# Optimization experiments

Hardware: AMD Instinct MI355X
Metric: run time of the kernel (lower is better)

## Reference

```python
import jax, jax.numpy as jnp
import numpy as np

BS, L, DIM = 16, 2048, 512
NUM_GROUPS, NUM_CODES = 2, 320
CODE_DIM = 256
VAR_DIM = CODE_DIM // NUM_GROUPS  # 128
INNER = DIM * 2                    # projFactor=2
TAU = 2.0                          # max(maxTemp*decay**0, minTemp) at numUpdates=0


def setup_inputs() -> dict:
    key = jax.random.key(0)
    ks = jax.random.split(key, 7)
    x = jax.random.normal(ks[0], (BS, L, DIM), jnp.float32)
    # gumbels = -log(Exp(1)) == standard Gumbel noise, matching torch's exponential_().log().neg()
    gumbels = jax.random.gumbel(ks[1], (BS * L * NUM_GROUPS, NUM_CODES), jnp.float32)
    W1 = jax.random.normal(ks[2], (DIM, INNER), jnp.float32) * (1.0 / np.sqrt(DIM))
    b1 = jnp.zeros((INNER,), jnp.float32)
    W2 = jax.random.normal(ks[3], (INNER, NUM_GROUPS * NUM_CODES), jnp.float32) * (1.0 / np.sqrt(INNER))
    b2 = jnp.zeros((NUM_GROUPS * NUM_CODES,), jnp.float32)
    # nn.init.uniform_ on embeddings: U[0,1); combineGroups=True -> single shared codebook (numCodes, varDim)
    emb = jax.random.uniform(ks[4], (NUM_CODES, VAR_DIM), jnp.float32)
    return {"x": x, "gumbels": gumbels, "W1": W1, "b1": b1, "W2": W2, "b2": b2, "emb": emb}


def reference(x, gumbels, W1, b1, W2, b2, emb):
    bs, l, d = x.shape
    xt = x.reshape(bs * l, d)
    h = jax.nn.gelu(xt @ W1 + b1, approximate=False)          # (N, INNER), torch GELU is exact erf
    logits = (h @ W2 + b2).reshape(bs * l * NUM_GROUPS, NUM_CODES)
    # training path: gumbel-softmax with straight-through hard one-hot
    soft = jax.nn.softmax((logits + gumbels) / TAU, axis=-1)  # (N*G, C)
    idx = jnp.argmax(soft, axis=-1)
    hard = jax.nn.one_hot(idx, NUM_CODES, dtype=soft.dtype)
    st = hard + soft - jax.lax.stop_gradient(soft)            # straight-through estimator
    st = st.reshape(bs * l, NUM_GROUPS, NUM_CODES)
    # combineGroups=True: embeddings repeated per group == shared codebook; the
    # (broadcast-mul).sum(-2) in torch is exactly this contraction (no huge intermediate).
    out = jnp.einsum('ngc,cd->ngd', st, emb)                  # (N, G, varDim)
    return out.reshape(bs, l, NUM_GROUPS * VAR_DIM)
```

## Files before the change

### kernel.cpp

```cpp
#include <hip/hip_runtime.h>
#include <math.h>


#define NTOK   32768
#define DIM    512
#define INNER  1024
#define NC     320
#define NGRP   2
#define VD     128
#define OUTD   256
#define RCAP   2048
#define MARGIN 8.0e-3f

#define L_LIST 16u
#define L_W1T  (64u<<10)
#define L_W2T  (2u<<20)
#define L_XH   (4u<<20)
#define L_H    (36u<<20)
#define L_PART (100u<<20)
#define L_HDW  (104u<<20)
#define WS_NEED (120u<<20)

#define W1F_OFF (1u<<20)
#define W2F_OFF (1u<<21)
#define SMEM_BYTES (65536 + 3328)

typedef _Float16 half8 __attribute__((ext_vector_type(8)));
typedef _Float16 half4 __attribute__((ext_vector_type(4)));
typedef float    f32x4 __attribute__((ext_vector_type(4)));

__device__ __forceinline__ float gelu_f(float s) {
  return 0.5f * s * (1.0f + erff(s * 0.70710678118654752440f));
}

#if defined(__has_builtin) && __has_builtin(__builtin_amdgcn_global_load_lds)
#define GLOAD16(gp, ldsbase) \
  __builtin_amdgcn_global_load_lds((const __attribute__((address_space(1))) void*)(gp), \
                                   (__attribute__((address_space(3))) void*)(ldsbase), 16, 0, 0)
#else
#define GLOAD16(gp, ldsbase) \
  do { *(uint4*)((char*)(ldsbase) + (threadIdx.x & 63) * 16) = *(const uint4*)(gp); } while (0)
#endif

#define XH_JOBS   2097152
#define W1T_JOBS  65536
#define W2T_JOBS  81920
#define PREP_JOBS (XH_JOBS + W1T_JOBS + W2T_JOBS)
__global__ __launch_bounds__(256)
void prep2_kernel(const float* __restrict__ x, const float* __restrict__ W1,
                  const float* __restrict__ W2, _Float16* __restrict__ xh,
                  _Float16* __restrict__ W1T, _Float16* __restrict__ W2T,
                  unsigned* __restrict__ cnt) {
  const int o = blockIdx.x * 256 + threadIdx.x;
  if (o == 0) cnt[0] = 0u;
  if (o < XH_JOBS) {
    const float4 v0 = *(const float4*)(x + (size_t)o * 8);
    const float4 v1 = *(const float4*)(x + (size_t)o * 8 + 4);
    half8 hv;
    hv[0] = (_Float16)v0.x; hv[1] = (_Float16)v0.y; hv[2] = (_Float16)v0.z; hv[3] = (_Float16)v0.w;
    hv[4] = (_Float16)v1.x; hv[5] = (_Float16)v1.y; hv[6] = (_Float16)v1.z; hv[7] = (_Float16)v1.w;
    *(half8*)(xh + (size_t)o * 8) = hv;
  } else if (o < XH_JOBS + W1T_JOBS) {
    const int q = o - XH_JOBS;
    const int i = q >> 6, k0 = (q & 63) * 8;
#pragma unroll
    for (int j = 0; j < 8; ++j)
      W1T[(size_t)i * DIM + k0 + j] = (_Float16)W1[(size_t)(k0 + j) * INNER + i];
  } else if (o < PREP_JOBS) {
    const int q = o - XH_JOBS - W1T_JOBS;
    const int c = q >> 7, i0 = (q & 127) * 8;
#pragma unroll
    for (int j = 0; j < 8; ++j)
      W2T[(size_t)c * INNER + i0 + j] = (_Float16)W2[(size_t)(i0 + j) * (NC * NGRP) + c];
  }
}

__global__ __launch_bounds__(256, 4)
void gemm1_kernel(const _Float16* __restrict__ xh, const _Float16* __restrict__ W1T,
                  const float* __restrict__ b1, _Float16* __restrict__ h) {
  __shared__ char smem[32768];
  const int tid = threadIdx.x;
  const int w = tid >> 6, l = tid & 63;
  const int l15 = l & 15, lq = l >> 4;
  const int bid = blockIdx.x;
  const int xcd = bid & 7, j = bid >> 3;
  const int bm = xcd * 32 + (j >> 3), bn = j & 7;
  const int wm = w >> 1, wn = w & 1;

  const int r0 = (w * 2 + 0) * 16 + (l >> 2);
  const int r1 = (w * 2 + 1) * 16 + (l >> 2);
  const int c0 = (((l & 3) ^ (r0 & 3)) * 8);
  const int c1 = (((l & 3) ^ (r1 & 3)) * 8);
  const _Float16* gA0 = xh  + (size_t)(bm * 128 + r0) * DIM + c0;
  const _Float16* gA1 = xh  + (size_t)(bm * 128 + r1) * DIM + c1;
  const _Float16* gB0 = W1T + (size_t)(bn * 128 + r0) * DIM + c0;
  const _Float16* gB1 = W1T + (size_t)(bn * 128 + r1) * DIM + c1;

#define STAGE_G(buf, ks) do { \
    char* b_ = smem + (buf) * 16384; \
    GLOAD16(gA0 + (ks) * 32, b_ + (w * 2 + 0) * 1024); \
    GLOAD16(gA1 + (ks) * 32, b_ + (w * 2 + 1) * 1024); \
    GLOAD16(gB0 + (ks) * 32, b_ + 8192 + (w * 2 + 0) * 1024); \
    GLOAD16(gB1 + (ks) * 32, b_ + 8192 + (w * 2 + 1) * 1024); \
  } while (0)

  f32x4 acc[4][4];
#pragma unroll
  for (int i = 0; i < 4; ++i)
#pragma unroll
    for (int jj = 0; jj < 4; ++jj) { f32x4 z = {0.f, 0.f, 0.f, 0.f}; acc[i][jj] = z; }

  const int swz = (lq ^ (l15 & 3)) << 4;
  const int aoff = (wm * 64 + l15) * 64 + swz;
  const int boff = 8192 + (wn * 64 + l15) * 64 + swz;

  STAGE_G(0, 0);
  __syncthreads();
  for (int ks = 0; ks < 16; ++ks) {
    const int cur = ks & 1;
    if (ks + 1 < 16) STAGE_G(cur ^ 1, ks + 1);
    const char* base = smem + cur * 16384;
    half8 a[4], b[4];
#pragma unroll
    for (int mi = 0; mi < 4; ++mi) a[mi] = *(const half8*)(base + aoff + mi * 1024);
#pragma unroll
    for (int ni = 0; ni < 4; ++ni) b[ni] = *(const half8*)(base + boff + ni * 1024);
#pragma unroll
    for (int mi = 0; mi < 4; ++mi)
#pragma unroll
      for (int ni = 0; ni < 4; ++ni)
        acc[mi][ni] = __builtin_amdgcn_mfma_f32_16x16x32_f16(a[mi], b[ni], acc[mi][ni], 0, 0, 0);
    __syncthreads();
  }

  _Float16* eT = (_Float16*)smem;
  float bb[4];
#pragma unroll
  for (int ni = 0; ni < 4; ++ni) bb[ni] = b1[bn * 128 + wn * 64 + ni * 16 + l15];
#pragma unroll
  for (int mi = 0; mi < 4; ++mi) {
    const int row = wm * 64 + mi * 16 + lq * 4;
#pragma unroll
    for (int ni = 0; ni < 4; ++ni) {
      const int col = (wn * 64 + ni * 16 + l15) ^ (lq << 4);
#pragma unroll
      for (int r = 0; r < 4; ++r)
        eT[(row + r) * 128 + col] = (_Float16)gelu_f(acc[mi][ni][r] + bb[ni]);
    }
  }
  __syncthreads();
#pragma unroll
  for (int it = 0; it < 8; ++it) {
    const int s = tid + it * 256;
    const int row = s >> 4, i8 = s & 15;
    const int colp = (i8 * 8) ^ (((row >> 2) & 3) << 4);
    *(half8*)(h + (size_t)(bm * 128 + row) * INNER + bn * 128 + i8 * 8)
        = *(const half8*)(eT + row * 128 + colp);
  }
}

__global__ __launch_bounds__(256, 4)
void gemm2_kernel(const _Float16* __restrict__ h, const _Float16* __restrict__ W2T,
                  const float* __restrict__ b2, const float* __restrict__ gum,
                  unsigned* __restrict__ part) {
  __shared__ char smem[32768];
  const int tid = threadIdx.x;
  const int w = tid >> 6, l = tid & 63;
  const int l15 = l & 15, lq = l >> 4;
  const int bid = blockIdx.x;
  const int xcd = bid & 7, j = bid >> 3;
  const int bm = xcd * 32 + j / 5, bt = j % 5;
  const int wm = w >> 1, wn = w & 1;

  const int r0 = (w * 2 + 0) * 16 + (l >> 2);
  const int r1 = (w * 2 + 1) * 16 + (l >> 2);
  const int c0 = (((l & 3) ^ (r0 & 3)) * 8);
  const int c1 = (((l & 3) ^ (r1 & 3)) * 8);
  const _Float16* gA0 = h   + (size_t)(bm * 128 + r0) * INNER + c0;
  const _Float16* gA1 = h   + (size_t)(bm * 128 + r1) * INNER + c1;
  const _Float16* gB0 = W2T + (size_t)(bt * 128 + r0) * INNER + c0;
  const _Float16* gB1 = W2T + (size_t)(bt * 128 + r1) * INNER + c1;

  f32x4 acc[4][4];
#pragma unroll
  for (int i = 0; i < 4; ++i)
#pragma unroll
    for (int jj = 0; jj < 4; ++jj) { f32x4 z = {0.f, 0.f, 0.f, 0.f}; acc[i][jj] = z; }

  const int swz = (lq ^ (l15 & 3)) << 4;
  const int aoff = (wm * 64 + l15) * 64 + swz;
  const int boff = 8192 + (wn * 64 + l15) * 64 + swz;

  STAGE_G(0, 0);
  __syncthreads();
  for (int ks = 0; ks < 32; ++ks) {
    const int cur = ks & 1;
    if (ks + 1 < 32) STAGE_G(cur ^ 1, ks + 1);
    const char* base = smem + cur * 16384;
    half8 a[4], b[4];
#pragma unroll
    for (int mi = 0; mi < 4; ++mi) a[mi] = *(const half8*)(base + aoff + mi * 1024);
#pragma unroll
    for (int ni = 0; ni < 4; ++ni) b[ni] = *(const half8*)(base + boff + ni * 1024);
#pragma unroll
    for (int mi = 0; mi < 4; ++mi)
#pragma unroll
      for (int ni = 0; ni < 4; ++ni)
        acc[mi][ni] = __builtin_amdgcn_mfma_f32_16x16x32_f16(a[mi], b[ni], acc[mi][ni], 0, 0, 0);
    __syncthreads();
  }

  float* eF = (float*)smem;
  const int nm = (bt == 2) ? 8 : 16;
#pragma unroll
  for (int half = 0; half < 2; ++half) {
    __syncthreads();
    if (wm == half) {
#pragma unroll
      for (int mi = 0; mi < 4; ++mi) {
        const int rl = mi * 16 + lq * 4;
#pragma unroll
        for (int ni = 0; ni < 4; ++ni) {
          const int col = (wn * 64 + ni * 16 + l15) ^ ((lq & 1) << 4);
#pragma unroll
          for (int r = 0; r < 4; ++r) eF[(rl + r) * 128 + col] = acc[mi][ni][r];
        }
      }
    }
    __syncthreads();
#pragma unroll
    for (int it = 0; it < 8; ++it) {
      const int s = tid + it * 256;
      const int rl = s >> 5, cc = (s & 31) * 4;
      const int ccp = cc ^ (((rl >> 2) & 1) << 4);
      const int t = bm * 128 + half * 64 + rl;
      const float4 lv  = *(const float4*)(eF + rl * 128 + ccp);
      const float4 b2v = *(const float4*)(b2 + bt * 128 + cc);
      const float4 gv  = *(const float4*)(gum + (size_t)t * 640 + bt * 128 + cc);
      float m1 = -1e30f, m2 = -1e30f; unsigned i1 = 0;
      const float vv[4] = {(lv.x + b2v.x) + gv.x, (lv.y + b2v.y) + gv.y,
                           (lv.z + b2v.z) + gv.z, (lv.w + b2v.w) + gv.w};
#pragma unroll
      for (int r = 0; r < 4; ++r) {
        const unsigned c = (unsigned)(bt * 128 + cc + r);
        if (vv[r] > m1) { m2 = m1; m1 = vv[r]; i1 = c; }
        else if (vv[r] > m2) m2 = vv[r];
      }
      for (int m = 1; m <= nm; m <<= 1) {
        const float om1 = __shfl_xor(m1, m);
        const float om2 = __shfl_xor(m2, m);
        const unsigned oi = (unsigned)__shfl_xor((int)i1, m);
        const bool take = (om1 > m1) || (om1 == m1 && oi < i1);
        if (take) { m2 = fmaxf(m1, om2); m1 = om1; i1 = oi; }
        else      { m2 = fmaxf(m2, om1); }
      }
      const int lr = tid & 31;
      const bool writer = (bt == 2) ? (lr == 0 || lr == 16) : (lr == 0);
      if (writer) {
        int slot;
        if (bt == 0) slot = 0; else if (bt == 1) slot = 1;
        else if (bt == 3) slot = 4; else if (bt == 4) slot = 5;
        else slot = (i1 < (unsigned)NC) ? 2 : 3;
        const unsigned ing = (i1 < (unsigned)NC) ? i1 : (i1 - NC);
        unsigned* p = part + ((size_t)t * 6 + slot) * 4;
        p[0] = __float_as_uint(m1);
        p[1] = __float_as_uint(m2);
        p[2] = ing;
      }
    }
  }
}

__global__ __launch_bounds__(256, 4)
void reduce_kernel(const unsigned* __restrict__ part, const float* __restrict__ emb,
                   float* __restrict__ out, unsigned* __restrict__ cnt,
                   unsigned* __restrict__ list) {
  __shared__ unsigned idxs[256];
  const int tid = threadIdx.x;
  const int pair = blockIdx.x * 256 + tid;
  const int t = pair >> 1, g = pair & 1;
  float m1 = -1e30f, m2 = -1e30f; unsigned i1 = 0;
#pragma unroll
  for (int s = 0; s < 3; ++s) {
    const unsigned* p = part + ((size_t)t * 6 + g * 3 + s) * 4;
    const float a1 = __uint_as_float(p[0]);
    const float a2 = __uint_as_float(p[1]);
    const unsigned ai = p[2];
    if (a1 > m1) { m2 = fmaxf(m1, a2); m1 = a1; i1 = ai; }
    else         { m2 = fmaxf(m2, a1); }
  }
  idxs[tid] = i1;
  if (m1 - m2 < MARGIN) {
    const unsigned pos = atomicAdd(cnt, 1u);
    if (pos < RCAP) list[pos] = (unsigned)((t << 1) | g);
  }
  __syncthreads();
#pragma unroll
  for (int it = 0; it < 32; ++it) {
    const int s2 = tid + it * 256;
    const int p = s2 >> 5, dd = (s2 & 31) * 4;
    *(float4*)(out + (size_t)blockIdx.x * 32768 + p * 128 + dd)
        = *(const float4*)(emb + (size_t)idxs[p] * VD + dd);
  }
}

__global__ __launch_bounds__(512, 4)
void refine1_kernel(const float* __restrict__ x, const float* __restrict__ W1,
                    const float* __restrict__ b1,
                    const unsigned* __restrict__ cnt, const unsigned* __restrict__ list,
                    float* __restrict__ hdws) {
  __shared__ float xs[DIM];
  unsigned n = cnt[0]; if (n > RCAP) n = RCAP;
  const unsigned e = blockIdx.x;
  if (e >= n) return;
  const unsigned tok = list[e] >> 1;
  const int tid = threadIdx.x;
  xs[tid] = x[(size_t)tok * DIM + tid];
  __syncthreads();
  double a0 = 0.0, a1 = 0.0, c0 = 0.0, c1 = 0.0;
#pragma unroll 4
  for (int k = 0; k < DIM; k += 2) {
    const double x0 = (double)xs[k], x1 = (double)xs[k + 1];
    const float* rr0 = W1 + (size_t)k * INNER + tid;
    const float* rr1 = W1 + (size_t)(k + 1) * INNER + tid;
    a0 += x0 * (double)rr0[0];
    a1 += x0 * (double)rr0[512];
    c0 += x1 * (double)rr1[0];
    c1 += x1 * (double)rr1[512];
  }
  const double s0 = a0 + c0 + (double)b1[tid];
  const double s1 = a1 + c1 + (double)b1[tid + 512];
  hdws[(size_t)e * INNER + tid]       = (float)(0.5 * s0 * (1.0 + erf(s0 * 0.70710678118654752440)));
  hdws[(size_t)e * INNER + tid + 512] = (float)(0.5 * s1 * (1.0 + erf(s1 * 0.70710678118654752440)));
}

__global__ __launch_bounds__(320, 4)
void refine2_kernel(const float* __restrict__ gum, const float* __restrict__ W2,
                    const float* __restrict__ b2, const float* __restrict__ emb,
                    float* __restrict__ out,
                    const unsigned* __restrict__ cnt, const unsigned* __restrict__ list,
                    const float* __restrict__ hdws) {
  __shared__ float hs[INNER];
  __shared__ double wv[5];
  __shared__ int wi[5];
  __shared__ int best;
  unsigned n = cnt[0]; if (n > RCAP) n = RCAP;
  const unsigned e = blockIdx.x;
  if (e >= n) return;
  const unsigned tok = list[e] >> 1;
  const int g = (int)(list[e] & 1u);
  const int tid = threadIdx.x;
  for (int j = tid; j < INNER; j += 320) hs[j] = hdws[(size_t)e * INNER + j];
  __syncthreads();
  const float* w2c = W2 + (size_t)g * NC + tid;
  double acc = 0.0, accb = 0.0;
#pragma unroll 4
  for (int k = 0; k < INNER; k += 2) {
    acc  += (double)hs[k]     * (double)w2c[(size_t)k * (NC * NGRP)];
    accb += (double)hs[k + 1] * (double)w2c[(size_t)(k + 1) * (NC * NGRP)];
  }
  double v = acc + accb + (double)b2[g * NC + tid]
                        + (double)gum[((size_t)tok * 2 + g) * NC + tid];
  int bi = tid;
#pragma unroll
  for (int m = 1; m < 64; m <<= 1) {
    const double ov = __shfl_xor(v, m);
    const int oi = __shfl_xor(bi, m);
    if (ov > v || (ov == v && oi < bi)) { v = ov; bi = oi; }
  }
  if ((tid & 63) == 0) { wv[tid >> 6] = v; wi[tid >> 6] = bi; }
  __syncthreads();
  if (tid == 0) {
    double bv = wv[0]; int bb = wi[0];
#pragma unroll
    for (int k = 1; k < 5; ++k)
      if (wv[k] > bv || (wv[k] == bv && wi[k] < bb)) { bv = wv[k]; bb = wi[k]; }
    best = bb;
  }
  __syncthreads();
  if (tid < VD)
    out[(size_t)tok * OUTD + g * VD + tid] = emb[(size_t)best * VD + tid];
}

#define W1F_N (16 * 64 * 64)
#define W2F_N (32 * 40 * 64)
__global__ void prep_kernel(const float* __restrict__ W1, const float* __restrict__ W2,
                            _Float16* __restrict__ W1F, _Float16* __restrict__ W2F,
                            unsigned* __restrict__ cnt) {
  const int o = blockIdx.x * 256 + threadIdx.x;
  if (o == 0) cnt[0] = 0u;
  if (o < W1F_N) {
    const int l = o & 63, ib = (o >> 6) & 63, ks = o >> 12;
    const int inner = ib * 16 + (l & 15);
    const int kb = ks * 32 + (l >> 4) * 8;
    _Float16* d = W1F + (size_t)o * 8;
#pragma unroll
    for (int j = 0; j < 8; ++j) d[j] = (_Float16)W1[(size_t)(kb + j) * INNER + inner];
  } else {
    const int o2 = o - W1F_N;
    if (o2 < W2F_N) {
      const int l = o2 & 63, cb = (o2 >> 6) % 40, ks = o2 / (40 * 64);
      const int code = cb * 16 + (l & 15);
      const int kb = ks * 32 + (l >> 4) * 8;
      _Float16* d = W2F + (size_t)o2 * 8;
#pragma unroll
      for (int j = 0; j < 8; ++j) d[j] = (_Float16)W2[(size_t)(kb + j) * (NC * NGRP) + code];
    }
  }
}

__global__ __launch_bounds__(512, 4)
void fused_kernel(const float* __restrict__ x, const float* __restrict__ gum,
                  const _Float16* __restrict__ W1F, const _Float16* __restrict__ W2F,
                  const float* __restrict__ b1, const float* __restrict__ b2,
                  const float* __restrict__ emb, float* __restrict__ out,
                  unsigned* __restrict__ cnt, unsigned* __restrict__ list) {
  extern __shared__ char smem[];
  float*    redm1 = (float*)(smem + 65536);
  float*    redm2 = (float*)(smem + 65536 + 1024);
  unsigned* redi  = (unsigned*)(smem + 65536 + 2048);
  unsigned* idxs  = (unsigned*)(smem + 65536 + 3072);
  const int tid = threadIdx.x;
  const int w = tid >> 6, l = tid & 63;
  const int l15 = l & 15, lq = l >> 4;
  const int T0 = blockIdx.x << 5;
#pragma unroll
  for (int i = 0; i < 8; ++i) {
    const int q = tid + i * 512;
    const int row = q >> 7;
    const int c = (q & 127) << 2;
    const float4 v = *(const float4*)(x + (size_t)(T0 + row) * DIM + c);
    half4 hv; hv[0] = (_Float16)v.x; hv[1] = (_Float16)v.y;
    hv[2] = (_Float16)v.z; hv[3] = (_Float16)v.w;
    const unsigned byte = ((unsigned)(row * 1024 + c * 2)) ^ ((unsigned)(row & 7) << 4);
    *(half4*)(smem + byte) = hv;
  }
  __syncthreads();
  {
    f32x4 acc[8][2];
#pragma unroll
    for (int i = 0; i < 8; ++i)
#pragma unroll
      for (int jj = 0; jj < 2; ++jj) { f32x4 z = {0.f,0.f,0.f,0.f}; acc[i][jj] = z; }
    const _Float16* w1f = W1F + (size_t)(w * 8) * 512 + (size_t)l * 8;
    for (int ks = 0; ks < 16; ++ks) {
      const int k0 = ks * 32;
      half8 a[8], bf[2];
#pragma unroll
      for (int mt = 0; mt < 8; ++mt) a[mt] = *(const half8*)(w1f + (size_t)(ks * 64 + mt) * 512);
#pragma unroll
      for (int nt = 0; nt < 2; ++nt) {
        const int token = nt * 16 + l15;
        const unsigned byte = ((unsigned)(token * 1024 + (k0 + lq * 8) * 2))
                              ^ ((unsigned)(token & 7) << 4);
        bf[nt] = *(const half8*)(smem + byte);
      }
#pragma unroll
      for (int mt = 0; mt < 8; ++mt)
#pragma unroll
        for (int nt = 0; nt < 2; ++nt)
          acc[mt][nt] = __builtin_amdgcn_mfma_f32_16x16x32_f16(a[mt], bf[nt], acc[mt][nt], 0, 0, 0);
    }
    __syncthreads();
#pragma unroll
    for (int mt = 0; mt < 8; ++mt) {
      const int inner0 = w * 128 + mt * 16 + lq * 4;
      const float4 bv = *(const float4*)(b1 + inner0);
#pragma unroll
      for (int nt = 0; nt < 2; ++nt) {
        const int token = nt * 16 + l15;
        const f32x4 v = acc[mt][nt];
        half4 hv;
        hv[0] = (_Float16)gelu_f(v[0] + bv.x);
        hv[1] = (_Float16)gelu_f(v[1] + bv.y);
        hv[2] = (_Float16)gelu_f(v[2] + bv.z);
        hv[3] = (_Float16)gelu_f(v[3] + bv.w);
        const unsigned byte = ((unsigned)(token * 2048 + inner0 * 2))
                              ^ ((unsigned)(token & 7) << 4);
        *(half4*)(smem + byte) = hv;
      }
    }
  }
  __syncthreads();
  const int g = w >> 2;
  {
    f32x4 acc[5][2];
#pragma unroll
    for (int i = 0; i < 5; ++i)
#pragma unroll
      for (int jj = 0; jj < 2; ++jj) { f32x4 z = {0.f,0.f,0.f,0.f}; acc[i][jj] = z; }
    const _Float16* w2f = W2F + (size_t)(w * 5) * 512 + (size_t)l * 8;
    for (int ks = 0; ks < 32; ++ks) {
      const int k0 = ks * 32;
      half8 a[5], bf[2];
#pragma unroll
      for (int mt = 0; mt < 5; ++mt) a[mt] = *(const half8*)(w2f + (size_t)(ks * 40 + mt) * 512);
#pragma unroll
      for (int nt = 0; nt < 2; ++nt) {
        const int token = nt * 16 + l15;
        const unsigned byte = ((unsigned)(token * 2048 + (k0 + lq * 8) * 2))
                              ^ ((unsigned)(token & 7) << 4);
        bf[nt] = *(const half8*)(smem + byte);
      }
#pragma unroll
      for (int mt = 0; mt < 5; ++mt)
#pragma unroll
        for (int nt = 0; nt < 2; ++nt)
          acc[mt][nt] = __builtin_amdgcn_mfma_f32_16x16x32_f16(a[mt], bf[nt], acc[mt][nt], 0, 0, 0);
    }
    float m1v[2] = {-1e30f,-1e30f};
    float m2v[2] = {-1e30f,-1e30f};
    unsigned i1v[2] = {0,0};
#pragma unroll
    for (int mt = 0; mt < 5; ++mt) {
      const int code0 = w * 80 + mt * 16 + lq * 4;
      const int cg0 = code0 - g * NC;
      const float4 b2v = *(const float4*)(b2 + code0);
#pragma unroll
      for (int nt = 0; nt < 2; ++nt) {
        const int tokg = T0 + nt * 16 + l15;
        const float4 gv = *(const float4*)(gum + ((size_t)tokg * 2 + g) * NC + cg0);
        const f32x4 v = acc[mt][nt];
        const float ss[4] = {v[0] + b2v.x + gv.x, v[1] + b2v.y + gv.y,
                             v[2] + b2v.z + gv.z, v[3] + b2v.w + gv.w};
#pragma unroll
        for (int r = 0; r < 4; ++r) {
          const float sv = ss[r];
          const unsigned cc = (unsigned)(cg0 + r);
          if (sv > m1v[nt]) { m2v[nt] = m1v[nt]; m1v[nt] = sv; i1v[nt] = cc; }
          else if (sv > m2v[nt]) m2v[nt] = sv;
        }
      }
    }
#pragma unroll
    for (int mask = 16; mask <= 32; mask <<= 1) {
#pragma unroll
      for (int nt = 0; nt < 2; ++nt) {
        const float om1 = __shfl_xor(m1v[nt], mask);
        const float om2 = __shfl_xor(m2v[nt], mask);
        const unsigned oi = (unsigned)__shfl_xor((int)i1v[nt], mask);
        const bool take = (om1 > m1v[nt]) || (om1 == m1v[nt] && oi < i1v[nt]);
        if (take) { m2v[nt] = fmaxf(m1v[nt], om2); m1v[nt] = om1; i1v[nt] = oi; }
        else      { m2v[nt] = fmaxf(m2v[nt], om1); }
      }
    }
    if (l < 16) {
#pragma unroll
      for (int nt = 0; nt < 2; ++nt) {
        const int tok = nt * 16 + l15;
        redm1[w * 32 + tok] = m1v[nt];
        redm2[w * 32 + tok] = m2v[nt];
        redi [w * 32 + tok] = i1v[nt];
      }
    }
  }
  __syncthreads();
  if (tid < 64) {
    const int pg = tid >> 5;
    const int tok = tid & 31;
    float m1 = -1e30f, m2 = -1e30f; unsigned i1 = 0;
#pragma unroll
    for (int k = 0; k < 4; ++k) {
      const int ww = pg * 4 + k;
      const float a1 = redm1[ww * 32 + tok];
      const float a2 = redm2[ww * 32 + tok];
      const unsigned ai = redi[ww * 32 + tok];
      if (a1 > m1) { m2 = fmaxf(m1, a2); m1 = a1; i1 = ai; }
      else         { m2 = fmaxf(m2, a1); }
    }
    idxs[tid] = i1;
    if (m1 - m2 < MARGIN) {
      const unsigned pos = atomicAdd(cnt, 1u);
      if (pos < RCAP) list[pos] = (unsigned)(((T0 + tok) << 1) | pg);
    }
  }
  __syncthreads();
#pragma unroll
  for (int i = 0; i < 4; ++i) {
    const int q = tid + i * 512;
    const int p = q >> 5;
    const int dd = q & 31;
    const int pg = p >> 5;
    const int tok = p & 31;
    const unsigned idx = idxs[p];
    *(float4*)(out + (size_t)(T0 + tok) * OUTD + pg * VD + dd * 4)
      = *(const float4*)(emb + (size_t)idx * VD + dd * 4);
  }
}

__global__ __launch_bounds__(512, 1)
void refine_kernel(const float* __restrict__ x, const float* __restrict__ gum,
                   const float* __restrict__ W1, const float* __restrict__ b1,
                   const float* __restrict__ W2, const float* __restrict__ b2,
                   const float* __restrict__ emb, float* __restrict__ out,
                   const unsigned* __restrict__ cnt, const unsigned* __restrict__ list) {
  __shared__ double xs[4][DIM];
  __shared__ double hd[4][INNER];
  __shared__ double sc[4][NC];
  __shared__ int amax[4];
  const int tid = threadIdx.x;
  unsigned n = cnt[0];
  if (n > RCAP) n = RCAP;
  for (unsigned base = blockIdx.x * 4u; base < n; base += gridDim.x * 4u) {
    const int nb = (int)((n - base) < 4u ? (n - base) : 4u);
    unsigned ng[4];
#pragma unroll
    for (int e = 0; e < 4; ++e) ng[e] = list[base + (e < nb ? e : 0)];
    for (int e = 0; e < nb; ++e)
      xs[e][tid] = (double)x[(size_t)(ng[e] >> 1) * DIM + tid];
    __syncthreads();
#pragma unroll
    for (int jj = 0; jj < 2; ++jj) {
      const int j = tid + jj * 512;
      double a0 = 0, a1 = 0, a2 = 0, a3 = 0;
      for (int k = 0; k < DIM; ++k) {
        const double wvv = (double)W1[(size_t)k * INNER + j];
        a0 += xs[0][k] * wvv; a1 += xs[1][k] * wvv;
        a2 += xs[2][k] * wvv; a3 += xs[3][k] * wvv;
      }
      const double bb = (double)b1[j];
      const double s0 = a0 + bb, s1 = a1 + bb, s2 = a2 + bb, s3 = a3 + bb;
      hd[0][j] = 0.5 * s0 * (1.0 + erf(s0 * 0.70710678118654752440));
      hd[1][j] = 0.5 * s1 * (1.0 + erf(s1 * 0.70710678118654752440));
      hd[2][j] = 0.5 * s2 * (1.0 + erf(s2 * 0.70710678118654752440));
      hd[3][j] = 0.5 * s3 * (1.0 + erf(s3 * 0.70710678118654752440));
    }
    __syncthreads();
    for (int task = tid; task < 4 * NC; task += 512) {
      const int e = task / NC;
      const int c = task - e * NC;
      if (e < nb) {
        const unsigned tok = ng[e] >> 1;
        const int gg = (int)(ng[e] & 1u);
        const float* w2c = W2 + (size_t)gg * NC + c;
        double acc = 0.0;
        for (int k = 0; k < INNER; ++k)
          acc += hd[e][k] * (double)w2c[(size_t)k * (NC * NGRP)];
        sc[e][c] = acc + (double)b2[gg * NC + c]
                       + (double)gum[((size_t)tok * 2 + gg) * NC + c];
      }
    }
    __syncthreads();
    if (tid < 4 && tid < nb) {
      double bestv = sc[tid][0]; int bi = 0;
      for (int c = 1; c < NC; ++c)
        if (sc[tid][c] > bestv) { bestv = sc[tid][c]; bi = c; }
      amax[tid] = bi;
    }
    __syncthreads();
    {
      const int e = tid >> 7;
      const int d = tid & 127;
      if (e < nb) {
        const unsigned tok = ng[e] >> 1;
        const int gg = (int)(ng[e] & 1u);
        out[(size_t)tok * OUTD + gg * VD + d] = emb[(size_t)amax[e] * VD + d];
      }
    }
    __syncthreads();
  }
}

extern "C" void kernel_launch(void* const* d_in, const int* in_sizes, int n_in,
                              void* d_out, int out_size, void* d_ws, size_t ws_size,
                              hipStream_t stream) {
  (void)in_sizes; (void)n_in; (void)out_size;
  const float* x   = (const float*)d_in[0];
  const float* gum = (const float*)d_in[1];
  const float* W1  = (const float*)d_in[2];
  const float* b1  = (const float*)d_in[3];
  const float* W2  = (const float*)d_in[4];
  const float* b2  = (const float*)d_in[5];
  const float* emb = (const float*)d_in[6];
  float* out = (float*)d_out;
  char* ws = (char*)d_ws;
  unsigned* cnt  = (unsigned*)ws;
  unsigned* list = (unsigned*)(ws + L_LIST);

  if (ws_size >= (size_t)WS_NEED) {
    _Float16* W1T = (_Float16*)(ws + L_W1T);
    _Float16* W2T = (_Float16*)(ws + L_W2T);
    _Float16* xh  = (_Float16*)(ws + L_XH);
    _Float16* h   = (_Float16*)(ws + L_H);
    unsigned* part = (unsigned*)(ws + L_PART);
    float* hdws = (float*)(ws + L_HDW);

    prep2_kernel<<<(PREP_JOBS + 255) / 256, 256, 0, stream>>>(x, W1, W2, xh, W1T, W2T, cnt);
    gemm1_kernel<<<(NTOK / 128) * 8, 256, 0, stream>>>(xh, W1T, b1, h);
    gemm2_kernel<<<(NTOK / 128) * 5, 256, 0, stream>>>(h, W2T, b2, gum, part);
    reduce_kernel<<<NTOK * NGRP / 256, 256, 0, stream>>>(part, emb, out, cnt, list);
    refine1_kernel<<<RCAP, 512, 0, stream>>>(x, W1, b1, cnt, list, hdws);
    refine2_kernel<<<RCAP, 320, 0, stream>>>(gum, W2, b2, emb, out, cnt, list, hdws);
  } else {
    _Float16* W1F = (_Float16*)(ws + W1F_OFF);
    _Float16* W2F = (_Float16*)(ws + W2F_OFF);
    hipFuncSetAttribute((const void*)fused_kernel,
                        hipFuncAttributeMaxDynamicSharedMemorySize, SMEM_BYTES);
    const int prep_items = W1F_N + W2F_N;
    prep_kernel<<<(prep_items + 255) / 256, 256, 0, stream>>>(W1, W2, W1F, W2F, cnt);
    fused_kernel<<<NTOK / 32, 512, SMEM_BYTES, stream>>>(x, gum, W1F, W2F, b1, b2,
                                                         emb, out, cnt, list);
    refine_kernel<<<256, 512, 0, stream>>>(x, gum, W1, b1, W2, b2, emb, out, cnt, list);
  }
}
```

Baseline: 314.1 us.

## Triple-buffer LDS staging in both GEMMs with one barrier per k-step

Both GEMM kernels move from double-buffered LDS to a three-stage ring. Loads are issued two k-steps ahead, and a manual vmcnt wait plus one barrier per iteration replaces the two implicit syncs, so global loads overlap MFMA work better. LDS per block grows from 32KB to 48KB, which may reduce the number of resident blocks per CU (launch bounds request 4). The hand-written waitcnt values depend on the exact number of outstanding loads, and the gemm2 epilogue relies on its own later __syncthreads.

```diff
diff --git a/kernel.cpp b/kernel.cpp
--- a/kernel.cpp
+++ b/kernel.cpp
@@ -41,6 +41,13 @@
 #define GLOAD16(gp, ldsbase) \
   do { *(uint4*)((char*)(ldsbase) + (threadIdx.x & 63) * 16) = *(const uint4*)(gp); } while (0)
 #endif
+
+#define PIPE_SYNC(N) do { \
+    __builtin_amdgcn_sched_barrier(0); \
+    asm volatile("s_waitcnt vmcnt(" #N ") lgkmcnt(0)" ::: "memory"); \
+    __builtin_amdgcn_s_barrier(); \
+    __builtin_amdgcn_sched_barrier(0); \
+  } while (0)
 
 #define XH_JOBS   2097152
 #define W1T_JOBS  65536
@@ -75,10 +82,18 @@
   }
 }
 
+#define STAGE_P(bufbase, ks) do { \
+    char* b_ = (bufbase); \
+    GLOAD16(gA0 + (ks) * 32, b_ + (w * 2 + 0) * 1024); \
+    GLOAD16(gA1 + (ks) * 32, b_ + (w * 2 + 1) * 1024); \
+    GLOAD16(gB0 + (ks) * 32, b_ + 8192 + (w * 2 + 0) * 1024); \
+    GLOAD16(gB1 + (ks) * 32, b_ + 8192 + (w * 2 + 1) * 1024); \
+  } while (0)
+
 __global__ __launch_bounds__(256, 4)
 void gemm1_kernel(const _Float16* __restrict__ xh, const _Float16* __restrict__ W1T,
                   const float* __restrict__ b1, _Float16* __restrict__ h) {
-  __shared__ char smem[32768];
+  __shared__ char smem[49152];
   const int tid = threadIdx.x;
   const int w = tid >> 6, l = tid & 63;
   const int l15 = l & 15, lq = l >> 4;
@@ -96,14 +111,6 @@
   const _Float16* gB0 = W1T + (size_t)(bn * 128 + r0) * DIM + c0;
   const _Float16* gB1 = W1T + (size_t)(bn * 128 + r1) * DIM + c1;
 
-#define STAGE_G(buf, ks) do { \
-    char* b_ = smem + (buf) * 16384; \
-    GLOAD16(gA0 + (ks) * 32, b_ + (w * 2 + 0) * 1024); \
-    GLOAD16(gA1 + (ks) * 32, b_ + (w * 2 + 1) * 1024); \
-    GLOAD16(gB0 + (ks) * 32, b_ + 8192 + (w * 2 + 0) * 1024); \
-    GLOAD16(gB1 + (ks) * 32, b_ + 8192 + (w * 2 + 1) * 1024); \
-  } while (0)
-
   f32x4 acc[4][4];
 #pragma unroll
   for (int i = 0; i < 4; ++i)
@@ -114,12 +121,13 @@
   const int aoff = (wm * 64 + l15) * 64 + swz;
   const int boff = 8192 + (wn * 64 + l15) * 64 + swz;
 
-  STAGE_G(0, 0);
-  __syncthreads();
+  STAGE_P(smem, 0);
+  asm volatile("" ::: "memory");
+  STAGE_P(smem + 16384, 1);
   for (int ks = 0; ks < 16; ++ks) {
-    const int cur = ks & 1;
-    if (ks + 1 < 16) STAGE_G(cur ^ 1, ks + 1);
-    const char* base = smem + cur * 16384;
+    if (ks + 1 < 16) PIPE_SYNC(4); else PIPE_SYNC(0);
+    if (ks + 2 < 16) STAGE_P(smem + ((ks + 2) % 3) * 16384, ks + 2);
+    const char* base = smem + (ks % 3) * 16384;
     half8 a[4], b[4];
 #pragma unroll
     for (int mi = 0; mi < 4; ++mi) a[mi] = *(const half8*)(base + aoff + mi * 1024);
@@ -130,8 +138,9 @@
 #pragma unroll
       for (int ni = 0; ni < 4; ++ni)
         acc[mi][ni] = __builtin_amdgcn_mfma_f32_16x16x32_f16(a[mi], b[ni], acc[mi][ni], 0, 0, 0);
-    __syncthreads();
-  }
+  }
+  asm volatile("s_waitcnt vmcnt(0) lgkmcnt(0)" ::: "memory");
+  __syncthreads();
 
   _Float16* eT = (_Float16*)smem;
   float bb[4];
@@ -163,7 +172,7 @@
 void gemm2_kernel(const _Float16* __restrict__ h, const _Float16* __restrict__ W2T,
                   const float* __restrict__ b2, const float* __restrict__ gum,
                   unsigned* __restrict__ part) {
-  __shared__ char smem[32768];
+  __shared__ char smem[49152];
   const int tid = threadIdx.x;
   const int w = tid >> 6, l = tid & 63;
   const int l15 = l & 15, lq = l >> 4;
@@ -191,12 +200,13 @@
   const int aoff = (wm * 64 + l15) * 64 + swz;
   const int boff = 8192 + (wn * 64 + l15) * 64 + swz;
 
-  STAGE_G(0, 0);
-  __syncthreads();
+  STAGE_P(smem, 0);
+  asm volatile("" ::: "memory");
+  STAGE_P(smem + 16384, 1);
   for (int ks = 0; ks < 32; ++ks) {
-    const int cur = ks & 1;
-    if (ks + 1 < 32) STAGE_G(cur ^ 1, ks + 1);
-    const char* base = smem + cur * 16384;
+    if (ks + 1 < 32) PIPE_SYNC(4); else PIPE_SYNC(0);
+    if (ks + 2 < 32) STAGE_P(smem + ((ks + 2) % 3) * 16384, ks + 2);
+    const char* base = smem + (ks % 3) * 16384;
     half8 a[4], b[4];
 #pragma unroll
     for (int mi = 0; mi < 4; ++mi) a[mi] = *(const half8*)(base + aoff + mi * 1024);
@@ -207,8 +217,8 @@
 #pragma unroll
       for (int ni = 0; ni < 4; ++ni)
         acc[mi][ni] = __builtin_amdgcn_mfma_f32_16x16x32_f16(a[mi], b[ni], acc[mi][ni], 0, 0, 0);
-    __syncthreads();
-  }
+  }
+  asm volatile("s_waitcnt vmcnt(0) lgkmcnt(0)" ::: "memory");
 
   float* eF = (float*)smem;
   const int nm = (bt == 2) ? 8 : 16;
```

After: 334.1 us. +6.4%, slower.
